# Kernel tuning notes

Measured on AMD Instinct MI355X. Metric: run time of the kernel, lower is better.

The kernel has to match this reference:

```python
import jax, jax.numpy as jnp
import numpy as np

T, E, B, D, N = 4, 4096, 2, 128, 384


def setup_inputs() -> dict:
    key = jax.random.key(0)
    ks = jax.random.split(key, 8)
    x = jax.random.normal(ks[0], (T, E, B, D), jnp.float32)
    feats = jax.random.normal(ks[1], (N, N, B, D), jnp.float32)
    # Node ids in [1, N]; id 0 is the padding row/col of the (N+1,N+1) grid.
    # Shared edge list across the batch (matches the repo's usage: the torch
    # scatter broadcasts one value over all batch slots, which is only
    # self-consistent when nodes are identical across batch).
    nodes1 = jax.random.randint(ks[2], (1, E, 2), 1, N + 1)
    nodes = jnp.broadcast_to(nodes1, (B, E, 2)).astype(jnp.int32)
    padding_mask = jnp.zeros((B, E), bool)
    padding_mask_feats = jnp.zeros((B, N), bool)
    pad = jax.random.normal(ks[3], (1,), jnp.float32)
    s1 = 1.0 / np.sqrt(D)
    s2 = 1.0 / np.sqrt(2 * D)
    W_g = jax.random.normal(ks[4], (D, D), jnp.float32) * s1
    b_g = jnp.zeros((D,), jnp.float32)
    W_lin = jax.random.normal(ks[5], (D, 2 * D), jnp.float32) * s2
    b_lin = jnp.zeros((D,), jnp.float32)
    W_f = jax.random.normal(ks[6], (D, D), jnp.float32) * s1
    b_f = jnp.zeros((D,), jnp.float32)
    return dict(x=x, feats=feats, nodes=nodes, padding_mask=padding_mask,
                padding_mask_feats=padding_mask_feats, pad=pad,
                W_g=W_g, b_g=b_g, W_lin=W_lin, b_lin=b_lin, W_f=W_f, b_f=b_f)


def _forward(x, feats, nodes, pad, W_g, b_g, W_lin, b_lin, W_f, b_f):
    # graph_layer stand-in: dense projection over embed dim
    x = jnp.einsum('tebd,od->tebo', x, W_g) + b_g            # (T,E,B,D)
    n_nodes, _, bsz, dim = feats.shape
    xmean = x.mean(0)                                        # (E,B,D)
    # dense padded (N+1,N+1,B,D) grid filled with learned pad value (faithful)
    grid = jnp.ones((n_nodes + 1, n_nodes + 1, bsz, dim), x.dtype) * pad
    n0 = nodes[0, :, 0]                                      # (E,) shared graph
    n1 = nodes[0, :, 1]
    grid = grid.at[n0, n1].set(xmean)                        # scatter edges into grid
    feats_update = grid[1:, 1:]                              # drop pad row/col -> (N,N,B,D)
    cat = jnp.concatenate([feats, feats_update], axis=-1)    # (N,N,B,2D)
    feats = jnp.einsum('nmbc,oc->nmbo', cat, W_lin) + b_lin  # Linear(2D -> D)
    # feat_layer stand-in: dense projection
    feats = jnp.einsum('nmbd,od->nmbo', feats, W_f) + b_f
    nodes_0 = jnp.maximum(nodes - 1, 0)                      # clamp after -1 shift
    g0 = nodes_0[:, :, 0].T                                  # (E,B)
    g1 = nodes_0[:, :, 1].T
    bidx = jnp.arange(bsz)[None, :]                          # (1,B)
    feats_subset = feats[g0, g1, bidx]                       # gather -> (E,B,D)
    x = x + feats_subset[None]                               # broadcast over trials
    return x, feats


def reference(x, feats, nodes, padding_mask, padding_mask_feats, pad,
              W_g, b_g, W_lin, b_lin, W_f, b_f):
    # padding masks are accepted for signature parity; the stub sub-layers
    # (single linear projections) do not consume them.
    return _forward(x, feats, nodes, pad, W_g, b_g, W_lin, b_lin, W_f, b_f)
```

## Files before the change

### kernel.cpp

```cpp
#include <hip/hip_runtime.h>
#include <hip/hip_bf16.h>


constexpr int T_ = 4, E_ = 4096, B_ = 2, D_ = 128, N_ = 384;
constexpr int EB = E_ * B_;
constexpr int XSTRIDE_T = E_ * B_ * D_;
constexpr int XROWS = T_ * EB;
constexpr int NROWS = N_ * N_ * B_;
constexpr int NCELLS = N_ * N_;

constexpr int WT0 = XROWS / 16;
constexpr int WT1 = EB / 16;
constexpr int WT2 = NROWS / 16;
constexpr int WTOT = WT0 + WT1 + WT2;

typedef __attribute__((ext_vector_type(8))) short bf16x8;
typedef __attribute__((ext_vector_type(4))) float f32x4;
union BF8 { bf16x8 v; ushort u[8]; };

constexpr size_t OFF_WTG    = 0;
constexpr size_t OFF_WTL    = 16384;
constexpr size_t OFF_WTR    = 32768;
constexpr size_t OFF_BCOMB  = 49152;
constexpr size_t OFF_BP     = 49280;
constexpr size_t OFF_XMEAN  = 49408;
constexpr size_t OFF_UC     = OFF_XMEAN + (size_t)EB * D_;
constexpr size_t OFF_WIN    = OFF_UC + (size_t)EB * D_;
constexpr size_t OFF_BPACK  = OFF_WIN + (size_t)NCELLS;
constexpr size_t OFF_BPACKG = OFF_BPACK + 16384;
constexpr size_t OFF_BPACKR = OFF_BPACKG + 16384;
constexpr size_t OFF_WGR    = OFF_BPACKR + 16384;
constexpr size_t OFF_BGR    = OFF_WGR + 16384;
constexpr size_t WS_FLOATS  = OFF_BGR + 128;

static __device__ inline ushort f2bf(float x) {
  const uint u = __float_as_uint(x);
  return (ushort)((u + 0x7fffu + ((u >> 16) & 1u)) >> 16);
}
static __device__ inline float bf2f(ushort h) {
  return __uint_as_float(((uint)h) << 16);
}

__global__ __launch_bounds__(256) void prep_kernel(
    const float* __restrict__ W_f, const float* __restrict__ W_lin,
    const float* __restrict__ W_g, const float* __restrict__ b_lin,
    const float* __restrict__ b_f, const float* __restrict__ pad,
    float* __restrict__ WtG, float* __restrict__ WtL, float* __restrict__ WtR,
    float* __restrict__ bcomb, float* __restrict__ bp, int* __restrict__ winner) {
  const int o = blockIdx.x;
  const int c = threadIdx.x;

  for (int i = blockIdx.x * 256 + c; i < NCELLS; i += 128 * 256) winner[i] = -1;

  float acc = 0.f;
#pragma unroll 4
  for (int d = 0; d < D_; ++d) acc += W_f[o * D_ + d] * W_lin[d * (2 * D_) + c];

  if (c < D_) {
    WtL[c * D_ + o] = acc;
    WtG[c * D_ + o] = W_g[o * D_ + c];
  } else {
    WtR[(c - D_) * D_ + o] = acc;
  }

  __shared__ float red[256];
  red[c] = (c >= D_) ? acc : 0.f;
  __syncthreads();
  for (int s = 128; s > 0; s >>= 1) {
    if (c < s) red[c] += red[c + s];
    __syncthreads();
  }
  const float padsum = red[0];
  __syncthreads();
  red[c] = (c < D_) ? W_f[o * D_ + c] * b_lin[c] : 0.f;
  __syncthreads();
  for (int s = 128; s > 0; s >>= 1) {
    if (c < s) red[c] += red[c + s];
    __syncthreads();
  }
  if (c == 0) {
    const float bc = b_f[o] + red[0];
    bcomb[o] = bc;
    bp[o] = bc + pad[0] * padsum;
  }
}

__global__ __launch_bounds__(128) void prepB_kernel(
    const float* __restrict__ WtR, const float* __restrict__ W_g,
    const float* __restrict__ b_g, float* __restrict__ Wgr_kn,
    float* __restrict__ bgr) {
  const int o = blockIdx.x;
  const int c = threadIdx.x;
  float acc = 0.f;
#pragma unroll 4
  for (int d = 0; d < D_; ++d) acc += WtR[d * D_ + o] * W_g[d * D_ + c];
  Wgr_kn[c * D_ + o] = acc;

  __shared__ float red[128];
  red[c] = WtR[c * D_ + o] * b_g[c];
  __syncthreads();
  for (int s = 64; s > 0; s >>= 1) {
    if (c < s) red[c] += red[c + s];
    __syncthreads();
  }
  if (c == 0) bgr[o] = red[0];
}

__global__ __launch_bounds__(64) void prep2_kernel(
    const float* __restrict__ W0, const float* __restrict__ W1,
    const float* __restrict__ W2, ushort* __restrict__ B0,
    ushort* __restrict__ B1, ushort* __restrict__ B2) {
  const float* Wkn = blockIdx.y == 0 ? W0 : (blockIdx.y == 1 ? W1 : W2);
  ushort* Bpack    = blockIdx.y == 0 ? B0 : (blockIdx.y == 1 ? B1 : B2);
  const int fi = blockIdx.x;
  const int l = threadIdx.x;
  const int ishi = (fi >> 5) ^ 1;
  const int k0 = (fi >> 3) & 3;
  const int n0 = fi & 7;
  const int o = n0 * 16 + (l & 15);
  const int kb = k0 * 32 + ((l >> 4) & 3) * 8;
  ushort* dst = Bpack + ((size_t)fi * 64 + l) * 8;
#pragma unroll
  for (int j = 0; j < 8; ++j) {
    const float w = Wkn[(size_t)(kb + j) * D_ + o];
    const ushort h = f2bf(w);
    if (ishi) {
      dst[j] = h;
    } else {
      dst[j] = f2bf(w - bf2f(h));
    }
  }
}

__global__ __launch_bounds__(256) void scatter_kernel(
    const int* __restrict__ nodes, int* __restrict__ winner) {
  const int e = blockIdx.x * 256 + threadIdx.x;
  if (e < E_) {
    const int n0 = nodes[e * 2 + 0];
    const int n1 = nodes[e * 2 + 1];
    atomicMax(&winner[(n0 - 1) * N_ + (n1 - 1)], e);
  }
}

__global__ __launch_bounds__(256) void mean_kernel(
    const float* __restrict__ x, float* __restrict__ xmean) {
  const int idx = blockIdx.x * 256 + threadIdx.x;
  const int pair = idx >> 5;
  const int o4 = (idx & 31) * 4;
  const size_t base = (size_t)pair * D_ + o4;
  float4 s = *(const float4*)&x[base];
  const float4 v1 = *(const float4*)&x[base + (size_t)1 * XSTRIDE_T];
  const float4 v2 = *(const float4*)&x[base + (size_t)2 * XSTRIDE_T];
  const float4 v3 = *(const float4*)&x[base + (size_t)3 * XSTRIDE_T];
  s.x = (s.x + v1.x + v2.x + v3.x) * 0.25f;
  s.y = (s.y + v1.y + v2.y + v3.y) * 0.25f;
  s.z = (s.z + v1.z + v2.z + v3.z) * 0.25f;
  s.w = (s.w + v1.w + v2.w + v3.w) * 0.25f;
  *(float4*)&xmean[base] = s;
}

__global__ __launch_bounds__(256) void mega_mfma_kernel(
    const float* __restrict__ x, const float* __restrict__ xmean,
    const float* __restrict__ feats,
    const ushort* __restrict__ BpG, const ushort* __restrict__ BpR,
    const ushort* __restrict__ BpL,
    const float* __restrict__ b_g, const float* __restrict__ bgr,
    const float* __restrict__ bpv,
    float* __restrict__ out_x, float* __restrict__ ucv,
    float* __restrict__ out_feats) {
  __shared__ float lw[4 * 2048];
  const int tid = threadIdx.x;
  const int wave = tid >> 6, lane = tid & 63;
  float* __restrict__ wlds = lw + wave * 2048;
  const int l15 = lane & 15;
  const int lh = (lane >> 4) & 3;
  const int asw = (l15 & 7) << 2;
  const int NW = gridDim.x * 4;

  int t = blockIdx.x * 4 + wave;
  float4 pf[8];
  {
    const float* As; int r0;
    if (t < WT0)            { As = x;     r0 = t * 16; }
    else if (t < WT0 + WT1) { As = xmean; r0 = (t - WT0) * 16; }
    else                    { As = feats; r0 = (t - WT0 - WT1) * 16; }
#pragma unroll
    for (int j = 0; j < 8; ++j) {
      const int idx = j * 64 + lane;
      pf[j] = *(const float4*)&As[((size_t)r0 + (idx >> 5)) * D_ + (idx & 31) * 4];
    }
  }

  for (; t < WTOT; t += NW) {
    const ushort* Bp; const float* bias; float* Dst; int r0;
    if (t < WT0)            { Bp = BpG; bias = b_g; Dst = out_x;     r0 = t * 16; }
    else if (t < WT0 + WT1) { Bp = BpR; bias = bgr; Dst = ucv;       r0 = (t - WT0) * 16; }
    else                    { Bp = BpL; bias = bpv; Dst = out_feats; r0 = (t - WT0 - WT1) * 16; }

#pragma unroll
    for (int j = 0; j < 8; ++j) {
      const int idx = j * 64 + lane;
      const int row = idx >> 5, c4 = idx & 31;
      *(float4*)&wlds[(row * 128 + c4 * 4) ^ ((row & 7) << 2)] = pf[j];
    }

    const int t2 = t + NW;
    if (t2 < WTOT) {
      const float* As; int r2;
      if (t2 < WT0)            { As = x;     r2 = t2 * 16; }
      else if (t2 < WT0 + WT1) { As = xmean; r2 = (t2 - WT0) * 16; }
      else                     { As = feats; r2 = (t2 - WT0 - WT1) * 16; }
#pragma unroll
      for (int j = 0; j < 8; ++j) {
        const int idx = j * 64 + lane;
        pf[j] = *(const float4*)&As[((size_t)r2 + (idx >> 5)) * D_ + (idx & 31) * 4];
      }
    }

    f32x4 acc[8];
#pragma unroll
    for (int n0 = 0; n0 < 8; ++n0) {
      const float b = bias[n0 * 16 + l15];
      acc[n0][0] = b; acc[n0][1] = b; acc[n0][2] = b; acc[n0][3] = b;
    }

    const bf16x8* __restrict__ bp8 = (const bf16x8*)Bp;
#pragma unroll
    for (int k0 = 0; k0 < 4; ++k0) {
      bf16x8 bh[8], bl[8];
#pragma unroll
      for (int n0 = 0; n0 < 8; ++n0) {
        bh[n0] = bp8[(size_t)((k0 * 8 + n0) * 64 + lane)];
        bl[n0] = bp8[(size_t)((32 + k0 * 8 + n0) * 64 + lane)];
      }
      const int base = l15 * 128 + lh * 8 + k0 * 32;
      const float4 a0 = *(const float4*)&wlds[(base + 0) ^ asw];
      const float4 a1 = *(const float4*)&wlds[(base + 4) ^ asw];
      const float xs[8] = {a0.x, a0.y, a0.z, a0.w, a1.x, a1.y, a1.z, a1.w};
      BF8 ah, al;
#pragma unroll
      for (int j = 0; j < 8; ++j) {
        const ushort h = f2bf(xs[j]);
        ah.u[j] = h;
        al.u[j] = f2bf(xs[j] - bf2f(h));
      }
#pragma unroll
      for (int n0 = 0; n0 < 8; ++n0) {
        acc[n0] = __builtin_amdgcn_mfma_f32_16x16x32_bf16(ah.v, bh[n0], acc[n0], 0, 0, 0);
        acc[n0] = __builtin_amdgcn_mfma_f32_16x16x32_bf16(al.v, bh[n0], acc[n0], 0, 0, 0);
        acc[n0] = __builtin_amdgcn_mfma_f32_16x16x32_bf16(ah.v, bl[n0], acc[n0], 0, 0, 0);
      }
    }

#pragma unroll
    for (int n0 = 0; n0 < 8; ++n0) {
      const int col = n0 * 16 + l15;
#pragma unroll
      for (int i = 0; i < 4; ++i) {
        const int row = lh * 4 + i;
        wlds[(row * 128 + col) ^ ((row & 7) << 2)] = acc[n0][i];
      }
    }
#pragma unroll
    for (int j = 0; j < 8; ++j) {
      const int idx = j * 64 + lane;
      const int row = idx >> 5, c4 = idx & 31;
      const float4 v =
          *(const float4*)&wlds[(row * 128 + c4 * 4) ^ ((row & 7) << 2)];
      *(float4*)&Dst[((size_t)r0 + row) * D_ + c4 * 4] = v;
    }
  }
}

__global__ __launch_bounds__(256) void fixup_kernel(
    const int* __restrict__ nodes, const int* __restrict__ winner,
    const float* __restrict__ uc, const float* __restrict__ bcomb,
    const float* __restrict__ bp, float* __restrict__ out_feats) {
  const int e = blockIdx.x;
  const int n0 = nodes[e * 2 + 0] - 1;
  const int n1 = nodes[e * 2 + 1] - 1;
  const int cell = n0 * N_ + n1;
  if (winner[cell] != e) return;
  const int t = threadIdx.x;
  const int b = t >> 7, o = t & 127;
  out_feats[((size_t)cell * 2 + b) * D_ + o] +=
      uc[((size_t)e * 2 + b) * D_ + o] + bcomb[o] - bp[o];
}

__global__ __launch_bounds__(256) void gather_add_kernel(
    const int* __restrict__ nodes, const float* __restrict__ out_feats,
    float* __restrict__ out_x) {
  const int e = blockIdx.x;
  const int tid = threadIdx.x;
  const int b = tid >> 7, o = tid & 127;
  const int n0 = nodes[((size_t)b * E_ + e) * 2 + 0] - 1;
  const int n1 = nodes[((size_t)b * E_ + e) * 2 + 1] - 1;
  const float fs = out_feats[(((size_t)n0 * N_ + n1) * B_ + b) * D_ + o];
#pragma unroll
  for (int t = 0; t < T_; ++t)
    out_x[(((size_t)t * E_ + e) * B_ + b) * D_ + o] += fs;
}

extern "C" void kernel_launch(void* const* d_in, const int* in_sizes, int n_in,
                              void* d_out, int out_size, void* d_ws, size_t ws_size,
                              hipStream_t stream) {
  const float* x      = (const float*)d_in[0];
  const float* feats  = (const float*)d_in[1];
  const int*   nodes  = (const int*)d_in[2];
  const float* pad    = (const float*)d_in[5];
  const float* W_g    = (const float*)d_in[6];
  const float* b_g    = (const float*)d_in[7];
  const float* W_lin  = (const float*)d_in[8];
  const float* b_lin  = (const float*)d_in[9];
  const float* W_f    = (const float*)d_in[10];
  const float* b_f    = (const float*)d_in[11];

  float* out_x     = (float*)d_out;
  float* out_feats = out_x + (size_t)T_ * E_ * B_ * D_;

  if (ws_size < WS_FLOATS * sizeof(float) + 16) return;

  float*  wsf    = (float*)d_ws;
  float*  WtG    = wsf + OFF_WTG;
  float*  WtL    = wsf + OFF_WTL;
  float*  WtR    = wsf + OFF_WTR;
  float*  bcomb  = wsf + OFF_BCOMB;
  float*  bpv    = wsf + OFF_BP;
  float*  xmean  = wsf + OFF_XMEAN;
  float*  uc     = wsf + OFF_UC;
  int*    win    = (int*)(wsf + OFF_WIN);
  ushort* Bpack  = (ushort*)(wsf + OFF_BPACK);
  ushort* BpackG = (ushort*)(wsf + OFF_BPACKG);
  ushort* BpackR = (ushort*)(wsf + OFF_BPACKR);
  float*  WgrKn  = wsf + OFF_WGR;
  float*  bgr    = wsf + OFF_BGR;

  prep_kernel<<<dim3(128), dim3(256), 0, stream>>>(W_f, W_lin, W_g, b_lin, b_f,
                                                   pad, WtG, WtL, WtR, bcomb,
                                                   bpv, win);
  prepB_kernel<<<dim3(128), dim3(128), 0, stream>>>(WtR, W_g, b_g, WgrKn, bgr);
  prep2_kernel<<<dim3(64, 3), dim3(64), 0, stream>>>(WtL, WtG, WgrKn, Bpack,
                                                     BpackG, BpackR);
  scatter_kernel<<<dim3(E_ / 256), dim3(256), 0, stream>>>(nodes, win);
  mean_kernel<<<dim3(EB * 32 / 256), dim3(256), 0, stream>>>(x, xmean);

  mega_mfma_kernel<<<dim3(1024), dim3(256), 0, stream>>>(
      x, xmean, feats, BpackG, BpackR, Bpack, b_g, bgr, bpv, out_x, uc,
      out_feats);
  fixup_kernel<<<dim3(E_), dim3(256), 0, stream>>>(nodes, win, uc, bcomb, bpv,
                                                   out_feats);
  gather_add_kernel<<<dim3(E_), dim3(256), 0, stream>>>(nodes, out_feats,
                                                        out_x);
}
```

Before: 443.8 us.

## Share 32-row tiles across block waves with split output columns

The persistent MFMA kernel now has all four waves of a block cooperate on one 32-row tile. Waves split the work into two row halves and two column halves, instead of each wave owning an independent 16-row tile. Each wave loads only half of the packed weight fragments, which cuts register pressure and weight traffic per wave. The change also adds launch_bounds occupancy hints and a strided block-to-tile remap. The cost is four block-wide barriers per tile and less independent overlap across waves.

Measured after the change: 419.6 us. 1.06x faster.

```diff
diff --git a/kernel.cpp b/kernel.cpp
--- a/kernel.cpp
+++ b/kernel.cpp
@@ -8,11 +8,6 @@
 constexpr int XROWS = T_ * EB;
 constexpr int NROWS = N_ * N_ * B_;
 constexpr int NCELLS = N_ * N_;
-
-constexpr int WT0 = XROWS / 16;
-constexpr int WT1 = EB / 16;
-constexpr int WT2 = NROWS / 16;
-constexpr int WTOT = WT0 + WT1 + WT2;
 
 typedef __attribute__((ext_vector_type(8))) short bf16x8;
 typedef __attribute__((ext_vector_type(4))) float f32x4;
@@ -159,7 +154,7 @@
   *(float4*)&xmean[base] = s;
 }
 
-__global__ __launch_bounds__(256) void mega_mfma_kernel(
+__global__ __launch_bounds__(256, 4) void mega2_kernel(
     const float* __restrict__ x, const float* __restrict__ xmean,
     const float* __restrict__ feats,
     const ushort* __restrict__ BpG, const ushort* __restrict__ BpR,
@@ -168,74 +163,80 @@
     const float* __restrict__ bpv,
     float* __restrict__ out_x, float* __restrict__ ucv,
     float* __restrict__ out_feats) {
-  __shared__ float lw[4 * 2048];
+  __shared__ float lw[4096];
   const int tid = threadIdx.x;
   const int wave = tid >> 6, lane = tid & 63;
-  float* __restrict__ wlds = lw + wave * 2048;
-  const int l15 = lane & 15;
-  const int lh = (lane >> 4) & 3;
-  const int asw = (l15 & 7) << 2;
-  const int NW = gridDim.x * 4;
-
-  int t = blockIdx.x * 4 + wave;
-  float4 pf[8];
+  const int l15 = lane & 15, lh = (lane >> 4) & 3;
+  const int rh = (wave & 1) * 16;
+  const int nb = (wave >> 1) * 4;
+  constexpr int GRID = 1024;
+  constexpr int TT0 = XROWS / 32;
+  constexpr int TT1 = EB / 32;
+  constexpr int TTOT = TT0 + TT1 + NROWS / 32;
+
+  const int bid = blockIdx.x;
+  int t = (bid & 7) * (GRID / 8) + (bid >> 3);
+
+  float4 pf[4];
   {
     const float* As; int r0;
-    if (t < WT0)            { As = x;     r0 = t * 16; }
-    else if (t < WT0 + WT1) { As = xmean; r0 = (t - WT0) * 16; }
-    else                    { As = feats; r0 = (t - WT0 - WT1) * 16; }
-#pragma unroll
-    for (int j = 0; j < 8; ++j) {
-      const int idx = j * 64 + lane;
-      pf[j] = *(const float4*)&As[((size_t)r0 + (idx >> 5)) * D_ + (idx & 31) * 4];
-    }
-  }
-
-  for (; t < WTOT; t += NW) {
+    if (t < TT0)            { As = x;     r0 = t * 32; }
+    else if (t < TT0 + TT1) { As = xmean; r0 = (t - TT0) * 32; }
+    else                    { As = feats; r0 = (t - TT0 - TT1) * 32; }
+#pragma unroll
+    for (int r = 0; r < 4; ++r) {
+      const int idx = r * 256 + tid;
+      pf[r] = *(const float4*)&As[((size_t)r0 + (idx >> 5)) * D_ + (idx & 31) * 4];
+    }
+  }
+
+  while (t < TTOT) {
     const ushort* Bp; const float* bias; float* Dst; int r0;
-    if (t < WT0)            { Bp = BpG; bias = b_g; Dst = out_x;     r0 = t * 16; }
-    else if (t < WT0 + WT1) { Bp = BpR; bias = bgr; Dst = ucv;       r0 = (t - WT0) * 16; }
-    else                    { Bp = BpL; bias = bpv; Dst = out_feats; r0 = (t - WT0 - WT1) * 16; }
-
-#pragma unroll
-    for (int j = 0; j < 8; ++j) {
-      const int idx = j * 64 + lane;
+    if (t < TT0)            { Bp = BpG; bias = b_g; Dst = out_x;     r0 = t * 32; }
+    else if (t < TT0 + TT1) { Bp = BpR; bias = bgr; Dst = ucv;       r0 = (t - TT0) * 32; }
+    else                    { Bp = BpL; bias = bpv; Dst = out_feats; r0 = (t - TT0 - TT1) * 32; }
+
+    __syncthreads();
+#pragma unroll
+    for (int r = 0; r < 4; ++r) {
+      const int idx = r * 256 + tid;
       const int row = idx >> 5, c4 = idx & 31;
-      *(float4*)&wlds[(row * 128 + c4 * 4) ^ ((row & 7) << 2)] = pf[j];
-    }
-
-    const int t2 = t + NW;
-    if (t2 < WTOT) {
+      *(float4*)&lw[(row * 128 + c4 * 4) ^ ((row & 7) << 2)] = pf[r];
+    }
+    const int tn = t + GRID;
+    if (tn < TTOT) {
       const float* As; int r2;
-      if (t2 < WT0)            { As = x;     r2 = t2 * 16; }
-      else if (t2 < WT0 + WT1) { As = xmean; r2 = (t2 - WT0) * 16; }
-      else                     { As = feats; r2 = (t2 - WT0 - WT1) * 16; }
-#pragma unroll
-      for (int j = 0; j < 8; ++j) {
-        const int idx = j * 64 + lane;
-        pf[j] = *(const float4*)&As[((size_t)r2 + (idx >> 5)) * D_ + (idx & 31) * 4];
-      }
-    }
-
-    f32x4 acc[8];
-#pragma unroll
-    for (int n0 = 0; n0 < 8; ++n0) {
-      const float b = bias[n0 * 16 + l15];
+      if (tn < TT0)            { As = x;     r2 = tn * 32; }
+      else if (tn < TT0 + TT1) { As = xmean; r2 = (tn - TT0) * 32; }
+      else                     { As = feats; r2 = (tn - TT0 - TT1) * 32; }
+#pragma unroll
+      for (int r = 0; r < 4; ++r) {
+        const int idx = r * 256 + tid;
+        pf[r] = *(const float4*)&As[((size_t)r2 + (idx >> 5)) * D_ + (idx & 31) * 4];
+      }
+    }
+    __syncthreads();
+
+    f32x4 acc[4];
+#pragma unroll
+    for (int n0 = 0; n0 < 4; ++n0) {
+      const float b = bias[(nb + n0) * 16 + l15];
       acc[n0][0] = b; acc[n0][1] = b; acc[n0][2] = b; acc[n0][3] = b;
     }
-
     const bf16x8* __restrict__ bp8 = (const bf16x8*)Bp;
 #pragma unroll
     for (int k0 = 0; k0 < 4; ++k0) {
-      bf16x8 bh[8], bl[8];
-#pragma unroll
-      for (int n0 = 0; n0 < 8; ++n0) {
-        bh[n0] = bp8[(size_t)((k0 * 8 + n0) * 64 + lane)];
-        bl[n0] = bp8[(size_t)((32 + k0 * 8 + n0) * 64 + lane)];
-      }
-      const int base = l15 * 128 + lh * 8 + k0 * 32;
-      const float4 a0 = *(const float4*)&wlds[(base + 0) ^ asw];
-      const float4 a1 = *(const float4*)&wlds[(base + 4) ^ asw];
+      bf16x8 bh[4], bl[4];
+#pragma unroll
+      for (int n0 = 0; n0 < 4; ++n0) {
+        bh[n0] = bp8[(size_t)((k0 * 8 + nb + n0) * 64 + lane)];
+        bl[n0] = bp8[(size_t)((32 + k0 * 8 + nb + n0) * 64 + lane)];
+      }
+      const int row = rh + l15;
+      const int fb = row * 128 + lh * 8 + k0 * 32;
+      const int sw = (row & 7) << 2;
+      const float4 a0 = *(const float4*)&lw[(fb + 0) ^ sw];
+      const float4 a1 = *(const float4*)&lw[(fb + 4) ^ sw];
       const float xs[8] = {a0.x, a0.y, a0.z, a0.w, a1.x, a1.y, a1.z, a1.w};
       BF8 ah, al;
 #pragma unroll
@@ -245,30 +246,33 @@
         al.u[j] = f2bf(xs[j] - bf2f(h));
       }
 #pragma unroll
-      for (int n0 = 0; n0 < 8; ++n0) {
+      for (int n0 = 0; n0 < 4; ++n0) {
         acc[n0] = __builtin_amdgcn_mfma_f32_16x16x32_bf16(ah.v, bh[n0], acc[n0], 0, 0, 0);
         acc[n0] = __builtin_amdgcn_mfma_f32_16x16x32_bf16(al.v, bh[n0], acc[n0], 0, 0, 0);
         acc[n0] = __builtin_amdgcn_mfma_f32_16x16x32_bf16(ah.v, bl[n0], acc[n0], 0, 0, 0);
       }
     }
-
-#pragma unroll
-    for (int n0 = 0; n0 < 8; ++n0) {
-      const int col = n0 * 16 + l15;
+    __syncthreads();
+
+#pragma unroll
+    for (int n0 = 0; n0 < 4; ++n0) {
+      const int col = (nb + n0) * 16 + l15;
 #pragma unroll
       for (int i = 0; i < 4; ++i) {
-        const int row = lh * 4 + i;
-        wlds[(row * 128 + col) ^ ((row & 7) << 2)] = acc[n0][i];
-      }
-    }
-#pragma unroll
-    for (int j = 0; j < 8; ++j) {
-      const int idx = j * 64 + lane;
+        const int row = rh + lh * 4 + i;
+        lw[(row * 128 + col) ^ ((row & 7) << 2)] = acc[n0][i];
+      }
+    }
+    __syncthreads();
+#pragma unroll
+    for (int r = 0; r < 4; ++r) {
+      const int idx = r * 256 + tid;
       const int row = idx >> 5, c4 = idx & 31;
       const float4 v =
-          *(const float4*)&wlds[(row * 128 + c4 * 4) ^ ((row & 7) << 2)];
+          *(const float4*)&lw[(row * 128 + c4 * 4) ^ ((row & 7) << 2)];
       *(float4*)&Dst[((size_t)r0 + row) * D_ + c4 * 4] = v;
     }
+    t = tn;
   }
 }
 
@@ -344,7 +348,7 @@
   scatter_kernel<<<dim3(E_ / 256), dim3(256), 0, stream>>>(nodes, win);
   mean_kernel<<<dim3(EB * 32 / 256), dim3(256), 0, stream>>>(x, xmean);
 
-  mega_mfma_kernel<<<dim3(1024), dim3(256), 0, stream>>>(
+  mega2_kernel<<<dim3(1024), dim3(256), 0, stream>>>(
       x, xmean, feats, BpackG, BpackR, Bpack, b_g, bgr, bpv, out_x, uc,
       out_feats);
   fixup_kernel<<<dim3(E_), dim3(256), 0, stream>>>(nodes, win, uc, bcomb, bpv,
```
